# Optimization experiments

Measured on AMD Instinct MI355X. Metric: run time of the kernel, lower is better.

The kernel has to match this reference:

```python
import jax, jax.numpy as jnp
import numpy as np

# CRPConfig defaults
KAPPA = 1.0
C = 0.95
ALPHA = 0.05
EPS = 1e-8
T_MAX = 32
MARGIN_FACTOR = 2.0

B, I, HD, L = 512, 1024, 2048, 1000


def setup_inputs() -> dict:
    key = jax.random.key(0)
    k0, k1, k2, k3 = jax.random.split(key, 4)
    x = jax.random.normal(k0, (B, I), jnp.float32)
    # kaiming-like scaling keeps activations numerically sane
    RIH = jax.random.normal(k1, (I, HD), jnp.float32) * np.float32(1.0 / np.sqrt(I))
    RH = jax.random.normal(k2, (HD, HD), jnp.float32) * np.float32(1.0 / np.sqrt(HD))
    RHL = jax.random.normal(k3, (HD, L), jnp.float32) * np.float32(1.0 / np.sqrt(HD))
    BH = jnp.zeros((HD,), jnp.float32)
    BL = jnp.zeros((L,), jnp.float32)
    MIH = jnp.ones((I, HD), jnp.float32)
    MH = jnp.ones((HD, HD), jnp.float32)
    MHL = jnp.ones((HD, L), jnp.float32)
    return {"x": x, "RIH": RIH, "RH": RH, "RHL": RHL, "BH": BH, "BL": BL,
            "MIH": MIH, "MH": MH, "MHL": MHL}


def _crp_forward(x, RIH, RH, RHL, BH, BL, MIH, MH, MHL):
    # build weights
    W_IH = RIH * MIH                      # [I, H]
    W_HL = RHL * MHL                      # [H, L]
    RHm = RH * MH                         # [H, H]
    # normalize so max column L1 <= c (value only; straight-through grad)
    col_l1 = jnp.abs(RHm).sum(axis=0)
    scale = C / jnp.maximum(col_l1.max(), EPS)
    W_H = jax.lax.stop_gradient(RHm * scale) + RHm - jax.lax.stop_gradient(RHm)

    rho = 1.0 - KAPPA + KAPPA * C
    denom = max(1e-12, 1.0 - rho)
    whl_inf = jnp.abs(W_HL).sum(axis=0).max()
    gamma_coef = whl_inf * (rho / denom)

    drive = x @ W_IH + BH                 # constant across steps, [B, H]
    Bsz = x.shape[0]
    Hs0 = jnp.zeros((Bsz, HD), x.dtype)
    active0 = jnp.ones((Bsz,), jnp.bool_)
    tau0 = jnp.full((Bsz,), T_MAX, jnp.int32)
    cert0 = jnp.zeros((Bsz,), jnp.bool_)
    logits_tau0 = jnp.zeros((Bsz, L), x.dtype)

    def step(carry, t):
        Hs, active, tau, certified, logits_tau = carry
        pre = Hs @ W_H + drive
        act = jnp.where(pre >= 0, pre, ALPHA * pre)      # LeakyReLU
        H_cand = (1.0 - KAPPA) * Hs + KAPPA * act
        H_next = jnp.where(active[:, None], H_cand, Hs)
        logits = H_next @ W_HL + BL
        # certification
        dH = jnp.max(jnp.abs(H_next - Hs), axis=1)       # H_prev == Hs
        Gamma = gamma_coef * dH
        top2 = jax.lax.top_k(logits, 2)[0]
        margin = top2[:, 0] - top2[:, 1]
        newly = active & (margin > MARGIN_FACTOR * Gamma)
        tau = jnp.where(newly, t, tau)
        certified = certified | newly
        logits_tau = jnp.where(newly[:, None], logits, logits_tau)
        active = active & (~newly)
        return (H_next, active, tau, certified, logits_tau), None

    ts = jnp.arange(1, T_MAX + 1, dtype=jnp.int32)
    (Hf, active, tau, certified, logits_tau), _ = jax.lax.scan(
        step, (Hs0, active0, tau0, cert0, logits_tau0), ts)

    never = ~certified
    logits_last = Hf @ W_HL + BL
    logits_tau = jnp.where(never[:, None], logits_last, logits_tau)
    return logits_tau


def reference(x, RIH, RH, RHL, BH, BL, MIH, MH, MHL):
    return _crp_forward(x, RIH, RH, RHL, BH, BL, MIH, MH, MHL)
```

## Files before the change

kernel.cpp:

```cpp
#include <hip/hip_runtime.h>

typedef __attribute__((ext_vector_type(8))) short short8;
typedef __attribute__((ext_vector_type(4))) float f32x4;

static constexpr int BN    = 512;
static constexpr int ID    = 1024;
static constexpr int HDm   = 2048;
static constexpr int LD    = 1000;
static constexpr int TMAXc = 32;
static constexpr float ALPHAc = 0.05f;

__device__ __forceinline__ unsigned short f2bf(float x) {
    unsigned u = __float_as_uint(x);
    u += 0x7fffu + ((u >> 16) & 1u);
    return (unsigned short)(u >> 16);
}
__device__ __forceinline__ float bf2f(unsigned short h) {
    return __uint_as_float(((unsigned)h) << 16);
}
__device__ __forceinline__ void split2(float x, unsigned short& hi, unsigned short& lo) {
    hi = f2bf(x);
    lo = f2bf(x - bf2f(hi));
}

template<bool SPLITA>
__device__ __forceinline__ void tile64x32(
    const float* __restrict__ Af,
    const unsigned short* __restrict__ Ahi, const unsigned short* __restrict__ Alo,
    int lda, int row0,
    const unsigned short* __restrict__ BThi, const unsigned short* __restrict__ BTlo,
    int ldk, int col0, int K, char* lds, f32x4& acc, int& s_out, int& p_out)
{
    char* Ah = lds;
    char* Al = lds + 16384;
    char* Bh = lds + 32768;
    char* Bl = lds + 40960;
    const int t = threadIdx.x, lane = t & 63, w = t >> 6;
    const int s = w & 7, p = w >> 3;
    s_out = s; p_out = p;
    f32x4 z = {0.f, 0.f, 0.f, 0.f};
    acc = z;

    const int ar = t >> 4, ac = (t & 15) << 3;
    const int br = t >> 5, bc = (t & 31) << 2;
    const int asb = (ar * 256 + ac * 2) ^ ((ar & 15) << 4);
    const int bsb = (br * 256 + bc * 2) ^ ((br & 15) << 4);
    const float* Ap = SPLITA ? (Af + (size_t)(row0 + ar) * lda + ac) : nullptr;
    const unsigned short* Ahp = SPLITA ? nullptr : (Ahi + (size_t)(row0 + ar) * lda + ac);
    const unsigned short* Alp = SPLITA ? nullptr : (Alo + (size_t)(row0 + ar) * lda + ac);
    const unsigned short* Bhp = BThi + (size_t)(col0 + br) * ldk + bc;
    const unsigned short* Blp = BTlo + (size_t)(col0 + br) * ldk + bc;

    const int frow = s >> 1, fcol = s & 1;
    const int arow = frow * 16 + (lane & 15);
    const int colr = fcol * 16 + (lane & 15);
    const int ab0 = arow * 256, bb0 = colr * 256;
    const int axor = (arow & 15) << 4, bxor = (colr & 15) << 4;
    const int kwin = p * 128 + ((lane >> 4) << 4);

    float4 af0a, af0b, af1a, af1b;
    uint4 ah0, al0, ah1, al1;
    if constexpr (SPLITA) {
        af0a = *(const float4*)(Ap);       af0b = *(const float4*)(Ap + 4);
        af1a = *(const float4*)(Ap + 128); af1b = *(const float4*)(Ap + 132);
    } else {
        ah0 = *(const uint4*)(Ahp);       al0 = *(const uint4*)(Alp);
        ah1 = *(const uint4*)(Ahp + 128); al1 = *(const uint4*)(Alp + 128);
    }
    uint2 bh0 = *(const uint2*)(Bhp),       bl0 = *(const uint2*)(Blp);
    uint2 bh1 = *(const uint2*)(Bhp + 128), bl1 = *(const uint2*)(Blp + 128);

    for (int k0 = 0; k0 < K; k0 += 128) {
        uint4 awh, awl;
        if constexpr (SPLITA) {
            unsigned short h[8], l[8];
            const float vv[8] = {af0a.x, af0a.y, af0a.z, af0a.w,
                                 af0b.x, af0b.y, af0b.z, af0b.w};
#pragma unroll
            for (int i = 0; i < 8; ++i) split2(vv[i], h[i], l[i]);
            awh = make_uint4((unsigned)h[0] | ((unsigned)h[1] << 16),
                             (unsigned)h[2] | ((unsigned)h[3] << 16),
                             (unsigned)h[4] | ((unsigned)h[5] << 16),
                             (unsigned)h[6] | ((unsigned)h[7] << 16));
            awl = make_uint4((unsigned)l[0] | ((unsigned)l[1] << 16),
                             (unsigned)l[2] | ((unsigned)l[3] << 16),
                             (unsigned)l[4] | ((unsigned)l[5] << 16),
                             (unsigned)l[6] | ((unsigned)l[7] << 16));
        } else { awh = ah0; awl = al0; }
        const uint2 bwh = bh0, bwl = bl0;
        __syncthreads();
        *(uint4*)(Ah + asb) = awh;
        *(uint4*)(Al + asb) = awl;
        *(uint2*)(Bh + bsb) = bwh;
        *(uint2*)(Bl + bsb) = bwl;
        if constexpr (SPLITA) { af0a = af1a; af0b = af1b; } else { ah0 = ah1; al0 = al1; }
        bh0 = bh1; bl0 = bl1;
        if (k0 + 256 < K) {
            if constexpr (SPLITA) {
                af1a = *(const float4*)(Ap + k0 + 256);
                af1b = *(const float4*)(Ap + k0 + 260);
            } else {
                ah1 = *(const uint4*)(Ahp + k0 + 256);
                al1 = *(const uint4*)(Alp + k0 + 256);
            }
            bh1 = *(const uint2*)(Bhp + k0 + 256);
            bl1 = *(const uint2*)(Blp + k0 + 256);
        }
        __syncthreads();
#pragma unroll
        for (int ks = 0; ks < 2; ++ks) {
            const int kb = kwin + ks * 64;
            short8 bh = *(const short8*)(Bh + ((bb0 + kb) ^ bxor));
            short8 bl = *(const short8*)(Bl + ((bb0 + kb) ^ bxor));
            short8 ah = *(const short8*)(Ah + ((ab0 + kb) ^ axor));
            short8 al = *(const short8*)(Al + ((ab0 + kb) ^ axor));
            acc = __builtin_amdgcn_mfma_f32_16x16x32_bf16(ah, bh, acc, 0, 0, 0);
            acc = __builtin_amdgcn_mfma_f32_16x16x32_bf16(al, bh, acc, 0, 0, 0);
            acc = __builtin_amdgcn_mfma_f32_16x16x32_bf16(ah, bl, acc, 0, 0, 0);
        }
    }
}

__device__ __forceinline__ void tile32x32(
    const unsigned short* __restrict__ Ahi, const unsigned short* __restrict__ Alo, int row0,
    const unsigned short* __restrict__ BThi, const unsigned short* __restrict__ BTlo,
    int col0, char* lds, f32x4& acc, int& s_out, int& p_out)
{
    char* Ah = lds;
    char* Al = lds + 8192;
    char* Bh = lds + 16384;
    char* Bl = lds + 24576;
    const int t = threadIdx.x, lane = t & 63, w = t >> 6;
    const int s = w & 3, p = w >> 2;
    s_out = s; p_out = p;
    f32x4 z = {0.f, 0.f, 0.f, 0.f};
    acc = z;

    const int ar = t >> 5, ac = (t & 31) << 2;
    const int asb = (ar * 256 + ac * 2) ^ ((ar & 15) << 4);
    const unsigned short* Ahp = Ahi + (size_t)(row0 + ar) * HDm + ac;
    const unsigned short* Alp = Alo + (size_t)(row0 + ar) * HDm + ac;
    const unsigned short* Bhp = BThi + (size_t)(col0 + ar) * HDm + ac;
    const unsigned short* Blp = BTlo + (size_t)(col0 + ar) * HDm + ac;

    const int frow = s >> 1, fcol = s & 1;
    const int arow = frow * 16 + (lane & 15);
    const int colr = fcol * 16 + (lane & 15);
    const int ab0 = arow * 256, bb0 = colr * 256;
    const int axor = (arow & 15) << 4, bxor = (colr & 15) << 4;
    const int kwin = p * 64 + ((lane >> 4) << 4);

    uint2 ah0 = *(const uint2*)(Ahp),       al0 = *(const uint2*)(Alp);
    uint2 bh0 = *(const uint2*)(Bhp),       bl0 = *(const uint2*)(Blp);
    uint2 ah1 = *(const uint2*)(Ahp + 128), al1 = *(const uint2*)(Alp + 128);
    uint2 bh1 = *(const uint2*)(Bhp + 128), bl1 = *(const uint2*)(Blp + 128);

    for (int k0 = 0; k0 < HDm; k0 += 128) {
        const uint2 awh = ah0, awl = al0, bwh = bh0, bwl = bl0;
        __syncthreads();
        *(uint2*)(Ah + asb) = awh;
        *(uint2*)(Al + asb) = awl;
        *(uint2*)(Bh + asb) = bwh;
        *(uint2*)(Bl + asb) = bwl;
        ah0 = ah1; al0 = al1; bh0 = bh1; bl0 = bl1;
        if (k0 + 256 < HDm) {
            ah1 = *(const uint2*)(Ahp + k0 + 256);
            al1 = *(const uint2*)(Alp + k0 + 256);
            bh1 = *(const uint2*)(Bhp + k0 + 256);
            bl1 = *(const uint2*)(Blp + k0 + 256);
        }
        __syncthreads();
        const int kb = kwin;
        short8 bh = *(const short8*)(Bh + ((bb0 + kb) ^ bxor));
        short8 bl = *(const short8*)(Bl + ((bb0 + kb) ^ bxor));
        short8 ah = *(const short8*)(Ah + ((ab0 + kb) ^ axor));
        short8 al = *(const short8*)(Al + ((ab0 + kb) ^ axor));
        acc = __builtin_amdgcn_mfma_f32_16x16x32_bf16(ah, bh, acc, 0, 0, 0);
        acc = __builtin_amdgcn_mfma_f32_16x16x32_bf16(al, bh, acc, 0, 0, 0);
        acc = __builtin_amdgcn_mfma_f32_16x16x32_bf16(ah, bl, acc, 0, 0, 0);
    }
}

__global__ void k_init(int* active, int* cnt, float* scal)
{
    int i = blockIdx.x * blockDim.x + threadIdx.x;
    if (i < 2 * BN) active[i] = 1;
    if (i < 16) cnt[i] = 64;
    if (i < 8) scal[i] = 0.f;
}

__global__ __launch_bounds__(256) void k_colsum_wh(const float* __restrict__ RH,
                                                   const float* __restrict__ MH,
                                                   float* __restrict__ part)
{
    const int colTile = blockIdx.x >> 3, rs = blockIdx.x & 7;
    const int col = colTile * 64 + (threadIdx.x & 63);
    const int rq = threadIdx.x >> 6;
    const int r0 = rs * 256;
    float s = 0.f;
    for (int i = r0 + rq; i < r0 + 256; i += 4)
        s += fabsf(RH[(size_t)i * HDm + col] * MH[(size_t)i * HDm + col]);
    __shared__ float red[4][64];
    red[rq][threadIdx.x & 63] = s;
    __syncthreads();
    if (threadIdx.x < 64)
        part[(size_t)rs * HDm + col] = red[0][threadIdx.x] + red[1][threadIdx.x] +
                                       red[2][threadIdx.x] + red[3][threadIdx.x];
}

__global__ __launch_bounds__(256) void k_colsum_whl(const float* __restrict__ RHL,
                                                    const float* __restrict__ MHL,
                                                    float* __restrict__ part)
{
    const int colTile = blockIdx.x >> 3, rs = blockIdx.x & 7;
    const int col = colTile * 64 + (threadIdx.x & 63);
    const int rq = threadIdx.x >> 6;
    const int r0 = rs * 256;
    float s = 0.f;
    if (col < LD) {
        for (int i = r0 + rq; i < r0 + 256; i += 4)
            s += fabsf(RHL[(size_t)i * LD + col] * MHL[(size_t)i * LD + col]);
    }
    __shared__ float red[4][64];
    red[rq][threadIdx.x & 63] = s;
    __syncthreads();
    if (threadIdx.x < 64)
        part[(size_t)rs * 1024 + col] = red[0][threadIdx.x] + red[1][threadIdx.x] +
                                        red[2][threadIdx.x] + red[3][threadIdx.x];
}

__global__ __launch_bounds__(1024) void k_scalars(const float* __restrict__ part_wh,
                                                  const float* __restrict__ part_whl,
                                                  float* scal)
{
    float m1 = 0.f, m2 = 0.f;
    for (int c = threadIdx.x; c < HDm; c += 1024) {
        float s = 0.f;
#pragma unroll
        for (int k = 0; k < 8; ++k) s += part_wh[(size_t)k * HDm + c];
        m1 = fmaxf(m1, s);
    }
    {
        const int c = threadIdx.x;
        if (c < 1024) {
            float s = 0.f;
#pragma unroll
            for (int k = 0; k < 8; ++k) s += part_whl[(size_t)k * 1024 + c];
            m2 = fmaxf(m2, s);
        }
    }
#pragma unroll
    for (int off = 1; off < 64; off <<= 1) {
        m1 = fmaxf(m1, __shfl_xor(m1, off));
        m2 = fmaxf(m2, __shfl_xor(m2, off));
    }
    __shared__ float r1[16], r2[16];
    if ((threadIdx.x & 63) == 0) { r1[threadIdx.x >> 6] = m1; r2[threadIdx.x >> 6] = m2; }
    __syncthreads();
    if (threadIdx.x == 0) {
        float a = 0.f, b = 0.f;
#pragma unroll
        for (int i = 0; i < 16; ++i) { a = fmaxf(a, r1[i]); b = fmaxf(b, r2[i]); }
        scal[2] = 0.95f / fmaxf(a, 1e-8f);
        scal[3] = b * 19.f;
    }
}

__global__ __launch_bounds__(256) void k_wsplit(
    const float* __restrict__ R, const float* __restrict__ M,
    unsigned short* __restrict__ Ohi, unsigned short* __restrict__ Olo,
    int NR, int NC, int NCp, const float* __restrict__ scal, int scidx)
{
    __shared__ float T[64][65];
    const int nct = NCp >> 6;
    const int c0 = (blockIdx.x % nct) << 6;
    const int r0 = (blockIdx.x / nct) << 6;
    const float s = (scidx >= 0) ? scal[scidx] : 1.f;
    const int t = threadIdx.x;
    const int ir = t >> 2, ics = (t & 3) << 4;
#pragma unroll
    for (int i = 0; i < 16; ++i) {
        const int c = c0 + ics + i;
        float v = 0.f;
        if (c < NC) {
            const size_t idx = (size_t)(r0 + ir) * NC + c;
            v = R[idx] * M[idx] * s;
        }
        T[ir][ics + i] = v;
    }
    __syncthreads();
    const int oc = t >> 2, ors = (t & 3) << 4;
    unsigned short hb[16], lb[16];
#pragma unroll
    for (int i = 0; i < 16; ++i) split2(T[ors + i][oc], hb[i], lb[i]);
    const size_t base = (size_t)(c0 + oc) * NR + r0 + ors;
    uint4 v;
    v.x = hb[0] | ((unsigned)hb[1] << 16);  v.y = hb[2] | ((unsigned)hb[3] << 16);
    v.z = hb[4] | ((unsigned)hb[5] << 16);  v.w = hb[6] | ((unsigned)hb[7] << 16);
    *(uint4*)(Ohi + base) = v;
    v.x = hb[8] | ((unsigned)hb[9] << 16);  v.y = hb[10] | ((unsigned)hb[11] << 16);
    v.z = hb[12] | ((unsigned)hb[13] << 16); v.w = hb[14] | ((unsigned)hb[15] << 16);
    *(uint4*)(Ohi + base + 8) = v;
    v.x = lb[0] | ((unsigned)lb[1] << 16);  v.y = lb[2] | ((unsigned)lb[3] << 16);
    v.z = lb[4] | ((unsigned)lb[5] << 16);  v.w = lb[6] | ((unsigned)lb[7] << 16);
    *(uint4*)(Olo + base) = v;
    v.x = lb[8] | ((unsigned)lb[9] << 16);  v.y = lb[10] | ((unsigned)lb[11] << 16);
    v.z = lb[12] | ((unsigned)lb[13] << 16); v.w = lb[14] | ((unsigned)lb[15] << 16);
    *(uint4*)(Olo + base + 8) = v;
}

__global__ __launch_bounds__(1024, 8) void k_drive_mfma(
    const float* __restrict__ x,
    const unsigned short* __restrict__ WIHThi, const unsigned short* __restrict__ WIHTlo,
    const float* __restrict__ BH, float* __restrict__ drive)
{
    __shared__ char lds[49152];
    f32x4 acc;
    int s, p;
    const int row0 = (blockIdx.x >> 6) * 64, col0 = (blockIdx.x & 63) * 32;
    tile64x32<true>(x, nullptr, nullptr, ID, row0, WIHThi, WIHTlo, ID, col0, ID,
                    lds, acc, s, p);
    const int lane = threadIdx.x & 63;
    __syncthreads();
    f32x4* red = (f32x4*)lds;
    if (p == 1) red[s * 64 + lane] = acc;
    __syncthreads();
    if (p == 0) {
        f32x4 o = red[s * 64 + lane];
        acc += o;
        const int frow = s >> 1, fcol = s & 1;
        const int gc = col0 + fcol * 16 + (lane & 15);
        const int gr0 = row0 + frow * 16 + ((lane >> 4) << 2);
        const float bh = BH[gc];
#pragma unroll
        for (int r = 0; r < 4; ++r)
            drive[(size_t)(gr0 + r) * HDm + gc] = acc[r] + bh;
    }
}

__global__ __launch_bounds__(1024, 8) void k_p1(
    const unsigned short* __restrict__ WHThi, const unsigned short* __restrict__ WHTlo,
    const float* __restrict__ drive,
    unsigned short* __restrict__ HAhi, unsigned short* __restrict__ HAlo,
    unsigned short* __restrict__ HBhi, unsigned short* __restrict__ HBlo,
    const float* __restrict__ logits, float* __restrict__ out,
    int* __restrict__ active, int* __restrict__ cnt, const float* __restrict__ scal,
    float* __restrict__ dhp, const float* __restrict__ m1p, const float* __restrict__ m2p,
    int t)
{
    __shared__ char lds[49152];
    __shared__ int sact[64], snew[64];
    __shared__ int s_cnt;
    const int pp = (t - 1) & 1, pc = t & 1;
    {
        const int* cp = cnt + pp * 8;
        int sum = 0;
#pragma unroll
        for (int i = 0; i < 8; ++i) sum += cp[i];
        if (sum == 0) return;
    }
    const int bid = blockIdx.x, tid = threadIdx.x;
    const int rt = bid >> 6, row0m = rt << 6, col0 = (bid & 63) * 32;
    const int* actP = active + pp * BN;
    int* actC = active + pc * BN;
    const unsigned short* Hshi = (t & 1) ? HAhi : HBhi;
    const unsigned short* Hslo = (t & 1) ? HAlo : HBlo;
    unsigned short* Hnhi = (t & 1) ? HBhi : HAhi;
    unsigned short* Hnlo = (t & 1) ? HBlo : HAlo;
    const float* dhpP = dhp + (size_t)pp * BN * 64;
    float* dhpC = dhp + (size_t)pc * BN * 64;

    if (t > 1) {
        const float gamma2 = 2.f * scal[3];
        const int rl = tid >> 4, j = tid & 15;
        const int r = row0m + rl;
        const int act = actP[r];
        float dh = fmaxf(fmaxf(dhpP[(size_t)r * 64 + j],      dhpP[(size_t)r * 64 + 16 + j]),
                         fmaxf(dhpP[(size_t)r * 64 + 32 + j], dhpP[(size_t)r * 64 + 48 + j]));
        float M1 = m1p[(size_t)r * 32 + j], M2 = m2p[(size_t)r * 32 + j];
        {
            float o1 = m1p[(size_t)r * 32 + 16 + j], o2 = m2p[(size_t)r * 32 + 16 + j];
            if (o1 > M1) { M2 = fmaxf(M1, o2); M1 = o1; }
            else M2 = fmaxf(M2, o1);
        }
#pragma unroll
        for (int off = 1; off < 16; off <<= 1) {
            dh = fmaxf(dh, __shfl_xor(dh, off));
            float o1 = __shfl_xor(M1, off), o2 = __shfl_xor(M2, off);
            if (o1 > M1) { M2 = fmaxf(M1, o2); M1 = o1; }
            else M2 = fmaxf(M2, o1);
        }
        if (j == 0) {
            int nw = act && ((M1 - M2) > gamma2 * dh);
            snew[rl] = nw;
            sact[rl] = act && !nw;
        }
    } else if (tid < 64) {
        sact[tid] = 1; snew[tid] = 0;
    }
    __syncthreads();
    if (tid < 64) {
        unsigned long long b = __ballot(sact[tid] != 0);
        actC[row0m + tid] = sact[tid];
        if (tid == 0) {
            s_cnt = __popcll(b);
            (cnt + pc * 8)[rt] = s_cnt;
        }
    }
    if (t > 1 && (bid & 63) == 0) {
        for (int rl2 = 0; rl2 < 64; ++rl2) {
            if (snew[rl2]) {
                const float* lr = logits + (size_t)(row0m + rl2) * LD;
                float* orow = out + (size_t)(row0m + rl2) * LD;
                for (int jj = tid; jj < LD; jj += 1024) orow[jj] = lr[jj];
            }
        }
    }
    __syncthreads();
    if (s_cnt == 0) return;

    f32x4 acc;
    int s, p;
    tile64x32<false>(nullptr, Hshi, Hslo, HDm, row0m, WHThi, WHTlo, HDm, col0, HDm,
                     lds, acc, s, p);
    const int lane = tid & 63;
    __syncthreads();
    f32x4* red = (f32x4*)lds;
    if (p == 1) red[s * 64 + lane] = acc;
    __syncthreads();
    float (*sdh)[2] = (float(*)[2])(lds + 16384);
    if (p == 0) {
        f32x4 o = red[s * 64 + lane];
        acc += o;
        const int frow = s >> 1, fcol = s & 1;
        const int gc = col0 + fcol * 16 + (lane & 15);
        const int gr0 = row0m + frow * 16 + ((lane >> 4) << 2);
        float dh4[4];
#pragma unroll
        for (int r = 0; r < 4; ++r) {
            const int gr = gr0 + r;
            const size_t idx = (size_t)gr * HDm + gc;
            const unsigned short oh = Hshi[idx], ol = Hslo[idx];
            const float old = bf2f(oh) + bf2f(ol);
            const int a = sact[gr - row0m];
            unsigned short nh, nl;
            if (a) {
                const float pre = acc[r] + drive[idx];
                const float av = pre >= 0.f ? pre : ALPHAc * pre;
                split2(av, nh, nl);
            } else { nh = oh; nl = ol; }
            Hnhi[idx] = nh; Hnlo[idx] = nl;
            dh4[r] = fabsf((bf2f(nh) + bf2f(nl)) - old);
        }
#pragma unroll
        for (int off = 1; off < 16; off <<= 1)
#pragma unroll
            for (int r = 0; r < 4; ++r)
                dh4[r] = fmaxf(dh4[r], __shfl_xor(dh4[r], off));
        if ((lane & 15) == 0) {
            const int rl0 = frow * 16 + ((lane >> 4) << 2);
#pragma unroll
            for (int r = 0; r < 4; ++r) sdh[rl0 + r][fcol] = dh4[r];
        }
    }
    __syncthreads();
    if (tid < 64) {
        float d = fmaxf(sdh[tid][0], sdh[tid][1]);
        dhpC[(size_t)(row0m + tid) * 64 + (bid & 63)] = d;
    }
}

__global__ __launch_bounds__(1024, 8) void k_p2(
    const unsigned short* __restrict__ WHLThi, const unsigned short* __restrict__ WHLTlo,
    const float* __restrict__ BL,
    const unsigned short* __restrict__ HAhi, const unsigned short* __restrict__ HAlo,
    const unsigned short* __restrict__ HBhi, const unsigned short* __restrict__ HBlo,
    float* __restrict__ logits, const int* __restrict__ active, const int* __restrict__ cnt,
    float* __restrict__ m1p, float* __restrict__ m2p, int t)
{
    __shared__ char lds[46080];
    __shared__ int s_any;
    const int pc = t & 1;
    {
        const int* cp = cnt + pc * 8;
        int sum = 0;
#pragma unroll
        for (int i = 0; i < 8; ++i) sum += cp[i];
        if (sum == 0) return;
    }
    const int bid = blockIdx.x, tid = threadIdx.x;
    const unsigned short* Hnhi = (t & 1) ? HBhi : HAhi;
    const unsigned short* Hnlo = (t & 1) ? HBlo : HAlo;
    const int* actC = active + pc * BN;
    const int row0 = (bid >> 5) * 32, col0 = (bid & 31) * 32;

    if (tid < 64) {
        int a = (tid < 32) ? actC[row0 + tid] : 0;
        unsigned long long bl = __ballot(a != 0);
        if (tid == 0) s_any = (bl != 0ull);
    }
    __syncthreads();
    if (!s_any) return;

    f32x4 acc;
    int s, p;
    tile32x32(Hnhi, Hnlo, row0, WHLThi, WHLTlo, col0, lds, acc, s, p);
    const int lane = tid & 63;
    __syncthreads();
    f32x4* red = (f32x4*)lds;
    if (p > 0) red[(p - 1) * 256 + s * 64 + lane] = acc;
    __syncthreads();
    float (*st1)[2] = (float(*)[2])(lds + 12288);
    float (*st2)[2] = (float(*)[2])(lds + 12544);
    if (p == 0) {
#pragma unroll
        for (int q = 0; q < 3; ++q) {
            f32x4 o = red[q * 256 + s * 64 + lane];
            acc += o;
        }
        const int frow = s >> 1, fcol = s & 1;
        const int gc = col0 + fcol * 16 + (lane & 15);
        const int gr0 = row0 + frow * 16 + ((lane >> 4) << 2);
        const bool okc = gc < LD;
        const float blv = okc ? BL[gc] : 0.f;
        float m1a[4], m2a[4];
#pragma unroll
        for (int r = 0; r < 4; ++r) {
            const float v = acc[r] + blv;
            if (okc) logits[(size_t)(gr0 + r) * LD + gc] = v;
            m1a[r] = okc ? v : -3.4e38f;
            m2a[r] = -3.4e38f;
        }
#pragma unroll
        for (int off = 1; off < 16; off <<= 1) {
#pragma unroll
            for (int r = 0; r < 4; ++r) {
                float o1 = __shfl_xor(m1a[r], off);
                float o2 = __shfl_xor(m2a[r], off);
                if (o1 > m1a[r]) { m2a[r] = fmaxf(m1a[r], o2); m1a[r] = o1; }
                else m2a[r] = fmaxf(m2a[r], o1);
            }
        }
        if ((lane & 15) == 0) {
            const int rl0 = frow * 16 + ((lane >> 4) << 2);
#pragma unroll
            for (int r = 0; r < 4; ++r) {
                st1[rl0 + r][fcol] = m1a[r];
                st2[rl0 + r][fcol] = m2a[r];
            }
        }
    }
    __syncthreads();
    if (tid < 32) {
        float M1 = st1[tid][0], M2 = st2[tid][0];
        {
            float o1 = st1[tid][1], o2 = st2[tid][1];
            if (o1 > M1) { M2 = fmaxf(M1, o2); M1 = o1; }
            else M2 = fmaxf(M2, o1);
        }
        m1p[(size_t)(row0 + tid) * 32 + (bid & 31)] = M1;
        m2p[(size_t)(row0 + tid) * 32 + (bid & 31)] = M2;
    }
}

__global__ __launch_bounds__(1024) void k_tail(
    const float* __restrict__ logits, const int* __restrict__ active,
    float* __restrict__ out)
{
    const int row0 = blockIdx.x * 64;
    for (int rl = 0; rl < 64; ++rl) {
        const int r = row0 + rl;
        if (active[r] && active[BN + r]) {
            const float* lr = logits + (size_t)r * LD;
            float* orow = out + (size_t)r * LD;
            for (int jj = threadIdx.x; jj < LD; jj += 1024) orow[jj] = lr[jj];
        }
    }
}

extern "C" void kernel_launch(void* const* d_in, const int* in_sizes, int n_in,
                              void* d_out, int out_size, void* d_ws, size_t ws_size,
                              hipStream_t stream)
{
    const float* x   = (const float*)d_in[0];
    const float* RIH = (const float*)d_in[1];
    const float* RH  = (const float*)d_in[2];
    const float* RHL = (const float*)d_in[3];
    const float* BH  = (const float*)d_in[4];
    const float* BL  = (const float*)d_in[5];
    const float* MIH = (const float*)d_in[6];
    const float* MH  = (const float*)d_in[7];
    const float* MHL = (const float*)d_in[8];
    float* out = (float*)d_out;
    char* w = (char*)d_ws;

    unsigned short* WHThi = (unsigned short*)(w);
    unsigned short* WHTlo = (unsigned short*)(w + 8388608);
    unsigned short* WXhi  = (unsigned short*)(w + 16777216);
    unsigned short* WXlo  = (unsigned short*)(w + 20971520);
    float* drive  = (float*)(w + 25165824);
    unsigned short* HAhi = (unsigned short*)(w + 29360128);
    unsigned short* HAlo = (unsigned short*)(w + 31457280);
    unsigned short* HBhi = (unsigned short*)(w + 33554432);
    unsigned short* HBlo = (unsigned short*)(w + 35651584);
    float* logits = (float*)(w + 37748736);
    float* scal   = (float*)(w + 39796736);
    int*   active = (int*)(w + 39796800);
    int*   cnt    = (int*)(w + 39800896);
    float* dhp    = (float*)(w + 39800960);
    float* m1p    = (float*)(w + 40063104);
    float* m2p    = (float*)(w + 40128640);

    k_init<<<4, 256, 0, stream>>>(active, cnt, scal);
    k_colsum_wh<<<256, 256, 0, stream>>>(RH, MH, dhp);
    k_colsum_whl<<<128, 256, 0, stream>>>(RHL, MHL, m1p);
    k_scalars<<<1, 1024, 0, stream>>>(dhp, m1p, scal);
    k_wsplit<<<512, 256, 0, stream>>>(RIH, MIH, WXhi, WXlo, ID, HDm, HDm, scal, -1);
    k_drive_mfma<<<512, 1024, 0, stream>>>(x, WXhi, WXlo, BH, drive);
    k_wsplit<<<1024, 256, 0, stream>>>(RH, MH, WHThi, WHTlo, HDm, HDm, HDm, scal, 2);
    k_wsplit<<<512, 256, 0, stream>>>(RHL, MHL, WXhi, WXlo, HDm, LD, 1024, scal, -1);
    (void)hipMemsetAsync(HAhi, 0, 4194304, stream);

    for (int t = 1; t <= TMAXc; ++t) {
        k_p1<<<512, 1024, 0, stream>>>(WHThi, WHTlo, drive, HAhi, HAlo, HBhi, HBlo,
                                       logits, out, active, cnt, scal, dhp, m1p, m2p, t);
        k_p2<<<512, 1024, 0, stream>>>(WXhi, WXlo, BL, HAhi, HAlo, HBhi, HBlo,
                                       logits, active, cnt, m1p, m2p, t);
    }
    k_tail<<<8, 1024, 0, stream>>>(logits, active, out);
}
```

Baseline: 1.518 ms.

## Skip logits GEMM for rows that provably cannot certify, deepen prefetch

Each row now carries its last computed margin and the accumulated hidden-state drift since then. A bound test in k_p2 skips the per-step logits GEMM for any block whose rows cannot pass the certification test this step. Freshness flags make k_p1 certify only rows whose logits were actually recomputed. The GEMM tile loop also moves from double to triple register prefetch of global operands, which costs extra registers. The skip relies on a hand-derived Lipschitz-style bound with a 0.99 slack factor and constants like 19 and 38, so an inexact bound could delay or miss certifications compared with the reference.

```diff
diff --git a/kernel.cpp b/kernel.cpp
--- a/kernel.cpp
+++ b/kernel.cpp
@@ -58,17 +58,20 @@
     const int axor = (arow & 15) << 4, bxor = (colr & 15) << 4;
     const int kwin = p * 128 + ((lane >> 4) << 4);
 
-    float4 af0a, af0b, af1a, af1b;
-    uint4 ah0, al0, ah1, al1;
+    float4 af0a, af0b, af1a, af1b, af2a, af2b;
+    uint4 ah0, al0, ah1, al1, ah2, al2;
     if constexpr (SPLITA) {
         af0a = *(const float4*)(Ap);       af0b = *(const float4*)(Ap + 4);
         af1a = *(const float4*)(Ap + 128); af1b = *(const float4*)(Ap + 132);
+        af2a = *(const float4*)(Ap + 256); af2b = *(const float4*)(Ap + 260);
     } else {
         ah0 = *(const uint4*)(Ahp);       al0 = *(const uint4*)(Alp);
         ah1 = *(const uint4*)(Ahp + 128); al1 = *(const uint4*)(Alp + 128);
+        ah2 = *(const uint4*)(Ahp + 256); al2 = *(const uint4*)(Alp + 256);
     }
     uint2 bh0 = *(const uint2*)(Bhp),       bl0 = *(const uint2*)(Blp);
     uint2 bh1 = *(const uint2*)(Bhp + 128), bl1 = *(const uint2*)(Blp + 128);
+    uint2 bh2 = *(const uint2*)(Bhp + 256), bl2 = *(const uint2*)(Blp + 256);
 
     for (int k0 = 0; k0 < K; k0 += 128) {
         uint4 awh, awl;
@@ -93,18 +96,19 @@
         *(uint4*)(Al + asb) = awl;
         *(uint2*)(Bh + bsb) = bwh;
         *(uint2*)(Bl + bsb) = bwl;
-        if constexpr (SPLITA) { af0a = af1a; af0b = af1b; } else { ah0 = ah1; al0 = al1; }
-        bh0 = bh1; bl0 = bl1;
-        if (k0 + 256 < K) {
+        if constexpr (SPLITA) { af0a = af1a; af0b = af1b; af1a = af2a; af1b = af2b; }
+        else { ah0 = ah1; al0 = al1; ah1 = ah2; al1 = al2; }
+        bh0 = bh1; bl0 = bl1; bh1 = bh2; bl1 = bl2;
+        if (k0 + 384 < K) {
             if constexpr (SPLITA) {
-                af1a = *(const float4*)(Ap + k0 + 256);
-                af1b = *(const float4*)(Ap + k0 + 260);
+                af2a = *(const float4*)(Ap + k0 + 384);
+                af2b = *(const float4*)(Ap + k0 + 388);
             } else {
-                ah1 = *(const uint4*)(Ahp + k0 + 256);
-                al1 = *(const uint4*)(Alp + k0 + 256);
+                ah2 = *(const uint4*)(Ahp + k0 + 384);
+                al2 = *(const uint4*)(Alp + k0 + 384);
             }
-            bh1 = *(const uint2*)(Bhp + k0 + 256);
-            bl1 = *(const uint2*)(Blp + k0 + 256);
+            bh2 = *(const uint2*)(Bhp + k0 + 384);
+            bl2 = *(const uint2*)(Blp + k0 + 384);
         }
         __syncthreads();
 #pragma unroll
@@ -181,10 +185,16 @@
     }
 }
 
-__global__ void k_init(int* active, int* cnt, float* scal)
+__global__ void k_init(int* active, int* cnt, float* scal,
+                       float* margS, float* drift, int* fresh)
 {
     int i = blockIdx.x * blockDim.x + threadIdx.x;
-    if (i < 2 * BN) active[i] = 1;
+    if (i < 2 * BN) {
+        active[i] = 1;
+        margS[i] = 3.4e38f;
+        drift[i] = 0.f;
+        fresh[i] = 1;
+    }
     if (i < 16) cnt[i] = 64;
     if (i < 8) scal[i] = 0.f;
 }
@@ -346,6 +356,7 @@
     const float* __restrict__ logits, float* __restrict__ out,
     int* __restrict__ active, int* __restrict__ cnt, const float* __restrict__ scal,
     float* __restrict__ dhp, const float* __restrict__ m1p, const float* __restrict__ m2p,
+    float* __restrict__ margS, float* __restrict__ drift, const int* __restrict__ fresh,
     int t)
 {
     __shared__ char lds[49152];
@@ -369,12 +380,18 @@
     unsigned short* Hnlo = (t & 1) ? HBlo : HAlo;
     const float* dhpP = dhp + (size_t)pp * BN * 64;
     float* dhpC = dhp + (size_t)pc * BN * 64;
+    const float* margSP = margS + pp * BN;
+    float* margSC = margS + pc * BN;
+    const float* driftP = drift + pp * BN;
+    float* driftC = drift + pc * BN;
+    const int* freshP = fresh + pp * BN;
 
     if (t > 1) {
         const float gamma2 = 2.f * scal[3];
         const int rl = tid >> 4, j = tid & 15;
         const int r = row0m + rl;
         const int act = actP[r];
+        const int fr = freshP[r];
         float dh = fmaxf(fmaxf(dhpP[(size_t)r * 64 + j],      dhpP[(size_t)r * 64 + 16 + j]),
                          fmaxf(dhpP[(size_t)r * 64 + 32 + j], dhpP[(size_t)r * 64 + 48 + j]));
         float M1 = m1p[(size_t)r * 32 + j], M2 = m2p[(size_t)r * 32 + j];
@@ -391,9 +408,12 @@
             else M2 = fmaxf(M2, o1);
         }
         if (j == 0) {
-            int nw = act && ((M1 - M2) > gamma2 * dh);
+            const float marg = M1 - M2;
+            int nw = fr && act && (marg > gamma2 * dh);
             snew[rl] = nw;
             sact[rl] = act && !nw;
+            margSC[r] = fr ? marg : margSP[r];
+            driftC[r] = fr ? 0.f : (driftP[r] + dh);
         }
     } else if (tid < 64) {
         sact[tid] = 1; snew[tid] = 0;
@@ -476,10 +496,13 @@
     const unsigned short* __restrict__ HAhi, const unsigned short* __restrict__ HAlo,
     const unsigned short* __restrict__ HBhi, const unsigned short* __restrict__ HBlo,
     float* __restrict__ logits, const int* __restrict__ active, const int* __restrict__ cnt,
-    float* __restrict__ m1p, float* __restrict__ m2p, int t)
+    float* __restrict__ m1p, float* __restrict__ m2p, const float* __restrict__ scal,
+    const float* __restrict__ dhp, const float* __restrict__ margS,
+    const float* __restrict__ drift, int* __restrict__ fresh, int t)
 {
     __shared__ char lds[46080];
-    __shared__ int s_any;
+    __shared__ int sposs[32];
+    __shared__ int s_go;
     const int pc = t & 1;
     {
         const int* cp = cnt + pc * 8;
@@ -492,15 +515,39 @@
     const unsigned short* Hnhi = (t & 1) ? HBhi : HAhi;
     const unsigned short* Hnlo = (t & 1) ? HBlo : HAlo;
     const int* actC = active + pc * BN;
+    const float* dhpC = dhp + (size_t)pc * BN * 64;
+    const float* margSc = margS + pc * BN;
+    const float* driftc = drift + pc * BN;
+    int* freshC = fresh + pc * BN;
     const int row0 = (bid >> 5) * 32, col0 = (bid & 31) * 32;
 
+    {
+        const int rr = tid >> 5, j = tid & 31;
+        const int r = row0 + rr;
+        float d = fmaxf(dhpC[(size_t)r * 64 + j], dhpC[(size_t)r * 64 + 32 + j]);
+#pragma unroll
+        for (int off = 1; off < 32; off <<= 1) d = fmaxf(d, __shfl_xor(d, off));
+        if (j == 0) {
+            const int act = actC[r];
+            int poss;
+            if (t == TMAXc) poss = act;
+            else {
+                const float whl = scal[3] * (1.f / 19.f);
+                poss = act && (margSc[r] + 2.f * whl * (driftc[r] + d) >
+                               0.99f * 38.f * whl * d);
+            }
+            sposs[rr] = poss;
+        }
+    }
+    __syncthreads();
     if (tid < 64) {
-        int a = (tid < 32) ? actC[row0 + tid] : 0;
-        unsigned long long bl = __ballot(a != 0);
-        if (tid == 0) s_any = (bl != 0ull);
-    }
-    __syncthreads();
-    if (!s_any) return;
+        int v = (tid < 32) ? sposs[tid] : 0;
+        unsigned long long b = __ballot(v != 0);
+        if (tid == 0) s_go = (b != 0ull);
+    }
+    __syncthreads();
+    if (tid < 32) freshC[row0 + tid] = s_go;
+    if (!s_go) return;
 
     f32x4 acc;
     int s, p;
@@ -610,8 +657,11 @@
     float* dhp    = (float*)(w + 39800960);
     float* m1p    = (float*)(w + 40063104);
     float* m2p    = (float*)(w + 40128640);
-
-    k_init<<<4, 256, 0, stream>>>(active, cnt, scal);
+    float* margS  = (float*)(w + 40194176);
+    float* drift  = (float*)(w + 40198272);
+    int*   fresh  = (int*)(w + 40202368);
+
+    k_init<<<4, 256, 0, stream>>>(active, cnt, scal, margS, drift, fresh);
     k_colsum_wh<<<256, 256, 0, stream>>>(RH, MH, dhp);
     k_colsum_whl<<<128, 256, 0, stream>>>(RHL, MHL, m1p);
     k_scalars<<<1, 1024, 0, stream>>>(dhp, m1p, scal);
@@ -623,9 +673,11 @@
 
     for (int t = 1; t <= TMAXc; ++t) {
         k_p1<<<512, 1024, 0, stream>>>(WHThi, WHTlo, drive, HAhi, HAlo, HBhi, HBlo,
-                                       logits, out, active, cnt, scal, dhp, m1p, m2p, t);
+                                       logits, out, active, cnt, scal, dhp, m1p, m2p,
+                                       margS, drift, fresh, t);
         k_p2<<<512, 1024, 0, stream>>>(WXhi, WXlo, BL, HAhi, HAlo, HBhi, HBlo,
-                                       logits, active, cnt, m1p, m2p, t);
+                                       logits, active, cnt, m1p, m2p, scal,
+                                       dhp, margS, drift, fresh, t);
     }
     k_tail<<<8, 1024, 0, stream>>>(logits, active, out);
 }
```

New measurement: 1.968 ms. 1.3x slower.
